# Performance work log

Hardware: AMD Instinct MI355X
Metric: run time of the kernel (lower is better)

The kernel has to match this reference:

```python
import jax, jax.numpy as jnp
import numpy as np

TEMP = 0.07  # module hardcodes self.temp = 0.07 regardless of ctor arg
N, C = 8192, 256


def setup_inputs() -> dict:
    key = jax.random.key(0)
    kq, kk = jax.random.split(key)
    q = jax.random.normal(kq, (N, C), dtype=jnp.float32)
    k = jax.random.normal(kk, (N, C), dtype=jnp.float32)
    return {"q": q, "k": k}


def reference(q, k):
    # Original builds logits = [l_pos, l_neg_row] per sample i where
    # l_pos = q_i . k_i and l_neg_row = q_i . k_j for j != i, then applies
    # CrossEntropyLoss with label 0. That logits row is exactly a permutation
    # of the full similarity row sim[i, :] = q_i @ k.T (diagonal = positive),
    # so CE(logits/T, 0) == logsumexp(sim_i/T) - sim_ii/T. Single fused GEMM
    # + row-wise logsumexp, identical math and gradients.
    sim = jnp.matmul(q, k.T) / TEMP            # [N, N]
    pos = jnp.diagonal(sim)                    # [N]
    lse = jax.nn.logsumexp(sim, axis=1)        # [N]
    return jnp.mean(lse - pos)                 # scalar loss
```

## Files before the change

kernel.cpp:

```cpp
#include <hip/hip_runtime.h>
#include <stdint.h>


#define N_ROWS 8192
#define C_DIM  256
#define BN     32
#define SPLIT  16
#define JCOLS  (N_ROWS / SPLIT)
#define JTILES (JCOLS / BN)
#define BLK_ROWS 128
#define TILE_B  (BN * C_DIM * 2)

typedef __attribute__((ext_vector_type(8)))  _Float16 half8;
typedef __attribute__((ext_vector_type(4)))  _Float16 half4;
typedef __attribute__((ext_vector_type(4)))  float    f32x4;

#if __has_builtin(__builtin_amdgcn_exp2f)
#define EXP2(x) __builtin_amdgcn_exp2f(x)
#else
#define EXP2(x) exp2f(x)
#endif
#if __has_builtin(__builtin_amdgcn_logf)
#define LOG2(x) __builtin_amdgcn_logf(x)
#else
#define LOG2(x) log2f(x)
#endif

__device__ __forceinline__ void gload_lds16(const void* g, void* l) {
  __builtin_amdgcn_global_load_lds(
      (const __attribute__((address_space(1))) unsigned int*)g,
      (__attribute__((address_space(3))) unsigned int*)l, 16, 0, 0);
}

__global__ void cvt_kernel(const float* __restrict__ q, const float* __restrict__ k,
                           _Float16* __restrict__ qh, _Float16* __restrict__ kh,
                           float* __restrict__ pP) {
  const float QS = 20.60992915555663f;
  int i = blockIdx.x * 256 + threadIdx.x;
  float4 qv = ((const float4*)q)[i];
  float4 kv = ((const float4*)k)[i];
  half4 qo, ko;
  qo[0] = (_Float16)(qv.x * QS); qo[1] = (_Float16)(qv.y * QS);
  qo[2] = (_Float16)(qv.z * QS); qo[3] = (_Float16)(qv.w * QS);
  ko[0] = (_Float16)kv.x; ko[1] = (_Float16)kv.y;
  ko[2] = (_Float16)kv.z; ko[3] = (_Float16)kv.w;
  ((half4*)qh)[i] = qo;
  ((half4*)kh)[i] = ko;

  float d = (float)qo[0] * (float)ko[0];
  d = fmaf((float)qo[1], (float)ko[1], d);
  d = fmaf((float)qo[2], (float)ko[2], d);
  d = fmaf((float)qo[3], (float)ko[3], d);
#pragma unroll
  for (int off = 1; off < 64; off <<= 1) d += __shfl_xor(d, off);
  if ((threadIdx.x & 63) == 0) pP[i >> 6] = d;
}

__launch_bounds__(256, 2)
__global__ void sim_lse_kernel(const _Float16* __restrict__ qh,
                               const _Float16* __restrict__ kh,
                               float* __restrict__ pM,
                               float* __restrict__ pS) {
  __shared__ __align__(16) _Float16 kt[2 * BN * C_DIM];
  const int tid  = threadIdx.x;
  const int lane = tid & 63;
  const int wave = tid >> 6;
  const int l15  = lane & 15;
  const int lg   = lane >> 4;

  const int bid  = blockIdx.x;
  const int sp   = bid & (SPLIT - 1);
  const int rb   = bid >> 4;
  const int row0 = rb * BLK_ROWS + wave * 32;

  half8 a[2][8];
#pragma unroll
  for (int rf = 0; rf < 2; ++rf) {
    const _Float16* qr = qh + (size_t)(row0 + rf * 16 + l15) * C_DIM + lg * 8;
#pragma unroll
    for (int ks = 0; ks < 8; ++ks) a[rf][ks] = *(const half8*)(qr + ks * 32);
  }

  float M[8], S[8];
#pragma unroll
  for (int s = 0; s < 8; ++s) { M[s] = -__builtin_inff(); S[s] = 0.f; }

  const int nl0 = l15;
  const int nl1 = 16 + l15;
  const int bb0 = nl0 * 512 + (((nl0 & 31) * 16) ^ (lg * 16));
  const int bb1 = nl1 * 512 + (((nl1 & 31) * 16) ^ (lg * 16));

  const char* ksrc = (const char*)(kh + (size_t)sp * JCOLS * C_DIM);
  char* lds = (char*)kt;

#pragma unroll
  for (int it = 0; it < 4; ++it) {
    int linear = it * 4096 + tid * 16;
    int row = linear >> 9;
    int gc  = ((linear >> 4) & 31) ^ (row & 31);
    gload_lds16(ksrc + row * 512 + gc * 16, lds + linear);
  }

  for (int jt = 0; jt < JTILES; ++jt) {
    __syncthreads();
    const char* cur = lds + (jt & 1) * TILE_B;

    if (jt + 1 < JTILES) {
      const char* src = ksrc + (size_t)(jt + 1) * TILE_B;
      char* nxt = lds + ((jt + 1) & 1) * TILE_B;
#pragma unroll
      for (int it = 0; it < 4; ++it) {
        int linear = it * 4096 + tid * 16;
        int row = linear >> 9;
        int gc  = ((linear >> 4) & 31) ^ (row & 31);
        gload_lds16(src + row * 512 + gc * 16, nxt + linear);
      }
    }

    f32x4 acc00 = {0.f,0.f,0.f,0.f}, acc01 = {0.f,0.f,0.f,0.f};
    f32x4 acc10 = {0.f,0.f,0.f,0.f}, acc11 = {0.f,0.f,0.f,0.f};

#pragma unroll
    for (int ks = 0; ks < 8; ++ks) {
      half8 b0 = *(const half8*)(cur + (bb0 ^ (ks * 64)));
      half8 b1 = *(const half8*)(cur + (bb1 ^ (ks * 64)));
      acc00 = __builtin_amdgcn_mfma_f32_16x16x32_f16(a[0][ks], b0, acc00, 0, 0, 0);
      acc01 = __builtin_amdgcn_mfma_f32_16x16x32_f16(a[0][ks], b1, acc01, 0, 0, 0);
      acc10 = __builtin_amdgcn_mfma_f32_16x16x32_f16(a[1][ks], b0, acc10, 0, 0, 0);
      acc11 = __builtin_amdgcn_mfma_f32_16x16x32_f16(a[1][ks], b1, acc11, 0, 0, 0);
    }

#pragma unroll
    for (int j = 0; j < 4; ++j) {
      {
        float v0 = acc00[j], v1 = acc01[j];
        float newM  = fmaxf(M[j], fmaxf(v0, v1));
        float alpha = EXP2(M[j] - newM);
        float p = EXP2(v0 - newM) + EXP2(v1 - newM);
        S[j] = fmaf(S[j], alpha, p);
        M[j] = newM;
      }
      {
        float v0 = acc10[j], v1 = acc11[j];
        float newM  = fmaxf(M[4 + j], fmaxf(v0, v1));
        float alpha = EXP2(M[4 + j] - newM);
        float p = EXP2(v0 - newM) + EXP2(v1 - newM);
        S[4 + j] = fmaf(S[4 + j], alpha, p);
        M[4 + j] = newM;
      }
    }
  }

#pragma unroll
  for (int s = 0; s < 8; ++s) {
#pragma unroll
    for (int off = 1; off < 16; off <<= 1) {
      float Mo = __shfl_xor(M[s], off);
      float So = __shfl_xor(S[s], off);
      float nm = fmaxf(M[s], Mo);
      S[s] = S[s] * EXP2(M[s] - nm) + So * EXP2(Mo - nm);
      M[s] = nm;
    }
  }

  if (l15 == 0) {
#pragma unroll
    for (int s = 0; s < 8; ++s) {
      int grow = row0 + (s >> 2) * 16 + lg * 4 + (s & 3);
      pM[(size_t)sp * N_ROWS + grow] = M[s];
      pS[(size_t)sp * N_ROWS + grow] = S[s];
    }
  }
}

__global__ void finish1_kernel(const float* __restrict__ pM, const float* __restrict__ pS,
                               const float* __restrict__ pP, float* __restrict__ pPart) {
  const int tid = threadIdx.x;
  const int r = blockIdx.x * 256 + tid;
  float m = -__builtin_inff();
#pragma unroll
  for (int s = 0; s < SPLIT; ++s) m = fmaxf(m, pM[s * N_ROWS + r]);
  float ssum = 0.f;
#pragma unroll
  for (int s = 0; s < SPLIT; ++s)
    ssum = fmaf(pS[s * N_ROWS + r], EXP2(pM[s * N_ROWS + r] - m), ssum);
  float accl = (m + LOG2(ssum)) - pP[r];
#pragma unroll
  for (int off = 1; off < 64; off <<= 1) accl += __shfl_xor(accl, off);
  __shared__ float wsum[4];
  if ((tid & 63) == 0) wsum[tid >> 6] = accl;
  __syncthreads();
  if (tid == 0)
    pPart[blockIdx.x] = wsum[0] + wsum[1] + wsum[2] + wsum[3];
}

__global__ void finish2_kernel(const float* __restrict__ pPart, float* __restrict__ out) {
  const int tid = threadIdx.x;
  float v = (tid < 32) ? pPart[tid] : 0.f;
#pragma unroll
  for (int off = 1; off < 64; off <<= 1) v += __shfl_xor(v, off);
  if (tid == 0)
    out[0] = v * (0.69314718055994531f / (float)N_ROWS);
}

extern "C" void kernel_launch(void* const* d_in, const int* in_sizes, int n_in,
                              void* d_out, int out_size, void* d_ws, size_t ws_size,
                              hipStream_t stream) {
  const float* q = (const float*)d_in[0];
  const float* k = (const float*)d_in[1];
  float* out = (float*)d_out;
  char* ws = (char*)d_ws;

  _Float16* qh = (_Float16*)ws;
  _Float16* kh = (_Float16*)(ws + (size_t)N_ROWS * C_DIM * 2);
  float* pM = (float*)(ws + (size_t)N_ROWS * C_DIM * 4);
  float* pS = pM + SPLIT * N_ROWS;
  float* pP = pS + SPLIT * N_ROWS;
  float* pPart = pP + N_ROWS;

  cvt_kernel<<<dim3(N_ROWS * C_DIM / 4 / 256), dim3(256), 0, stream>>>(q, k, qh, kh, pP);
  sim_lse_kernel<<<dim3((N_ROWS / BLK_ROWS) * SPLIT), dim3(256), 0, stream>>>(qh, kh, pM, pS);
  finish1_kernel<<<dim3(N_ROWS / 256), dim3(256), 0, stream>>>(pM, pS, pP, pPart);
  finish2_kernel<<<dim3(1), dim3(64), 0, stream>>>(pPart, out);
}
```

Measured before the change: 112.6 us.

## Triple-buffer K tiles in LDS with prefetch distance two and partial vmcnt waits

Grows the LDS ring for K tiles from two to three buffers and issues global-to-LDS loads two tiles ahead. Explicit s_waitcnt vmcnt(4) plus a raw s_barrier replace __syncthreads, so each iteration waits only for the oldest tile's loads. The goal is to hide global load latency behind the MFMA and LSE work. LDS use rises from 32KB to 48KB per block, which could cut occupancy below the two blocks per CU the launch bounds request. The hand-written waitcnt is also fragile if the compiler emits other vector memory ops.

```diff
diff --git a/kernel.cpp b/kernel.cpp
--- a/kernel.cpp
+++ b/kernel.cpp
@@ -10,6 +10,7 @@
 #define JTILES (JCOLS / BN)
 #define BLK_ROWS 128
 #define TILE_B  (BN * C_DIM * 2)
+#define NBUF   3
 
 typedef __attribute__((ext_vector_type(8)))  _Float16 half8;
 typedef __attribute__((ext_vector_type(4)))  _Float16 half4;
@@ -61,7 +62,7 @@
                                const _Float16* __restrict__ kh,
                                float* __restrict__ pM,
                                float* __restrict__ pS) {
-  __shared__ __align__(16) _Float16 kt[2 * BN * C_DIM];
+  __shared__ __align__(16) _Float16 kt[NBUF * BN * C_DIM];
   const int tid  = threadIdx.x;
   const int lane = tid & 63;
   const int wave = tid >> 6;
@@ -93,29 +94,38 @@
   const char* ksrc = (const char*)(kh + (size_t)sp * JCOLS * C_DIM);
   char* lds = (char*)kt;
 
-#pragma unroll
-  for (int it = 0; it < 4; ++it) {
-    int linear = it * 4096 + tid * 16;
-    int row = linear >> 9;
-    int gc  = ((linear >> 4) & 31) ^ (row & 31);
-    gload_lds16(ksrc + row * 512 + gc * 16, lds + linear);
-  }
-
+#define STAGE(t, bufidx)                                                     \
+  do {                                                                       \
+    const char* _src = ksrc + (size_t)(t) * TILE_B;                          \
+    char* _dst = lds + (bufidx) * TILE_B;                                    \
+    _Pragma("unroll")                                                        \
+    for (int _it = 0; _it < 4; ++_it) {                                      \
+      int _lin = _it * 4096 + tid * 16;                                      \
+      int _row = _lin >> 9;                                                  \
+      int _gc  = ((_lin >> 4) & 31) ^ (_row & 31);                           \
+      gload_lds16(_src + _row * 512 + _gc * 16, _dst + _lin);                \
+    }                                                                        \
+  } while (0)
+
+  STAGE(0, 0);
+  STAGE(1, 1);
+
+  int cb = 0;
   for (int jt = 0; jt < JTILES; ++jt) {
-    __syncthreads();
-    const char* cur = lds + (jt & 1) * TILE_B;
-
-    if (jt + 1 < JTILES) {
-      const char* src = ksrc + (size_t)(jt + 1) * TILE_B;
-      char* nxt = lds + ((jt + 1) & 1) * TILE_B;
-#pragma unroll
-      for (int it = 0; it < 4; ++it) {
-        int linear = it * 4096 + tid * 16;
-        int row = linear >> 9;
-        int gc  = ((linear >> 4) & 31) ^ (row & 31);
-        gload_lds16(src + row * 512 + gc * 16, nxt + linear);
-      }
-    }
+    if (jt < JTILES - 1) {
+      asm volatile("s_waitcnt vmcnt(4)" ::: "memory");
+    } else {
+      asm volatile("s_waitcnt vmcnt(0)" ::: "memory");
+    }
+    __builtin_amdgcn_sched_barrier(0);
+    __builtin_amdgcn_s_barrier();
+
+    if (jt + 2 < JTILES) {
+      int nb = cb + 2; if (nb >= NBUF) nb -= NBUF;
+      STAGE(jt + 2, nb);
+    }
+
+    const char* cur = lds + cb * TILE_B;
 
     f32x4 acc00 = {0.f,0.f,0.f,0.f}, acc01 = {0.f,0.f,0.f,0.f};
     f32x4 acc10 = {0.f,0.f,0.f,0.f}, acc11 = {0.f,0.f,0.f,0.f};
@@ -149,7 +159,10 @@
         M[4 + j] = newM;
       }
     }
-  }
+
+    ++cb; if (cb >= NBUF) cb -= NBUF;
+  }
+#undef STAGE
 
 #pragma unroll
   for (int s = 0; s < 8; ++s) {
```

Result: no change. 110.9 us (-1.6%).

## Load K tiles directly from global into registers, dropping LDS staging

Applied to the files above, without the earlier changes.

Replaces the double-buffered LDS staging of K tiles (global_load_lds plus __syncthreads) with direct per-wave global half8 loads into registers, each followed by a batch of MFMAs raised in priority with s_setprio. This removes LDS traffic and block-wide barriers. In exchange each of the four waves now fetches the same K data separately from L2/L1 with no prefetch pipelining, so load latency is exposed unless occupancy hides it.

```diff
diff --git a/kernel.cpp b/kernel.cpp
--- a/kernel.cpp
+++ b/kernel.cpp
@@ -25,12 +25,6 @@
 #else
 #define LOG2(x) log2f(x)
 #endif
-
-__device__ __forceinline__ void gload_lds16(const void* g, void* l) {
-  __builtin_amdgcn_global_load_lds(
-      (const __attribute__((address_space(1))) unsigned int*)g,
-      (__attribute__((address_space(3))) unsigned int*)l, 16, 0, 0);
-}
 
 __global__ void cvt_kernel(const float* __restrict__ q, const float* __restrict__ k,
                            _Float16* __restrict__ qh, _Float16* __restrict__ kh,
@@ -61,7 +55,6 @@
                                const _Float16* __restrict__ kh,
                                float* __restrict__ pM,
                                float* __restrict__ pS) {
-  __shared__ __align__(16) _Float16 kt[2 * BN * C_DIM];
   const int tid  = threadIdx.x;
   const int lane = tid & 63;
   const int wave = tid >> 6;
@@ -85,56 +78,45 @@
 #pragma unroll
   for (int s = 0; s < 8; ++s) { M[s] = -__builtin_inff(); S[s] = 0.f; }
 
-  const int nl0 = l15;
-  const int nl1 = 16 + l15;
-  const int bb0 = nl0 * 512 + (((nl0 & 31) * 16) ^ (lg * 16));
-  const int bb1 = nl1 * 512 + (((nl1 & 31) * 16) ^ (lg * 16));
-
-  const char* ksrc = (const char*)(kh + (size_t)sp * JCOLS * C_DIM);
-  char* lds = (char*)kt;
-
-#pragma unroll
-  for (int it = 0; it < 4; ++it) {
-    int linear = it * 4096 + tid * 16;
-    int row = linear >> 9;
-    int gc  = ((linear >> 4) & 31) ^ (row & 31);
-    gload_lds16(ksrc + row * 512 + gc * 16, lds + linear);
-  }
+  const char* kb0 = (const char*)(kh + (size_t)sp * JCOLS * C_DIM)
+                    + l15 * 512 + lg * 16;
+  const char* kb1 = kb0 + 16 * 512;
 
   for (int jt = 0; jt < JTILES; ++jt) {
-    __syncthreads();
-    const char* cur = lds + (jt & 1) * TILE_B;
-
-    if (jt + 1 < JTILES) {
-      const char* src = ksrc + (size_t)(jt + 1) * TILE_B;
-      char* nxt = lds + ((jt + 1) & 1) * TILE_B;
-#pragma unroll
-      for (int it = 0; it < 4; ++it) {
-        int linear = it * 4096 + tid * 16;
-        int row = linear >> 9;
-        int gc  = ((linear >> 4) & 31) ^ (row & 31);
-        gload_lds16(src + row * 512 + gc * 16, nxt + linear);
-      }
-    }
-
     f32x4 acc00 = {0.f,0.f,0.f,0.f}, acc01 = {0.f,0.f,0.f,0.f};
     f32x4 acc10 = {0.f,0.f,0.f,0.f}, acc11 = {0.f,0.f,0.f,0.f};
 
-#pragma unroll
-    for (int ks = 0; ks < 8; ++ks) {
-      half8 b0 = *(const half8*)(cur + (bb0 ^ (ks * 64)));
-      half8 b1 = *(const half8*)(cur + (bb1 ^ (ks * 64)));
-      acc00 = __builtin_amdgcn_mfma_f32_16x16x32_f16(a[0][ks], b0, acc00, 0, 0, 0);
-      acc01 = __builtin_amdgcn_mfma_f32_16x16x32_f16(a[0][ks], b1, acc01, 0, 0, 0);
-      acc10 = __builtin_amdgcn_mfma_f32_16x16x32_f16(a[1][ks], b0, acc10, 0, 0, 0);
-      acc11 = __builtin_amdgcn_mfma_f32_16x16x32_f16(a[1][ks], b1, acc11, 0, 0, 0);
-    }
+    {
+      half8 b[8];
+#pragma unroll
+      for (int ks = 0; ks < 8; ++ks) b[ks] = *(const half8*)(kb0 + ks * 64);
+      __builtin_amdgcn_s_setprio(1);
+#pragma unroll
+      for (int ks = 0; ks < 8; ++ks) {
+        acc00 = __builtin_amdgcn_mfma_f32_16x16x32_f16(a[0][ks], b[ks], acc00, 0, 0, 0);
+        acc10 = __builtin_amdgcn_mfma_f32_16x16x32_f16(a[1][ks], b[ks], acc10, 0, 0, 0);
+      }
+      __builtin_amdgcn_s_setprio(0);
+    }
+    {
+      half8 b[8];
+#pragma unroll
+      for (int ks = 0; ks < 8; ++ks) b[ks] = *(const half8*)(kb1 + ks * 64);
+      __builtin_amdgcn_s_setprio(1);
+#pragma unroll
+      for (int ks = 0; ks < 8; ++ks) {
+        acc01 = __builtin_amdgcn_mfma_f32_16x16x32_f16(a[0][ks], b[ks], acc01, 0, 0, 0);
+        acc11 = __builtin_amdgcn_mfma_f32_16x16x32_f16(a[1][ks], b[ks], acc11, 0, 0, 0);
+      }
+      __builtin_amdgcn_s_setprio(0);
+    }
+    kb0 += TILE_B; kb1 += TILE_B;
 
 #pragma unroll
     for (int j = 0; j < 4; ++j) {
       {
         float v0 = acc00[j], v1 = acc01[j];
-        float newM  = fmaxf(M[j], fmaxf(v0, v1));
+        float newM  = fmaxf(fmaxf(M[j], v0), v1);
         float alpha = EXP2(M[j] - newM);
         float p = EXP2(v0 - newM) + EXP2(v1 - newM);
         S[j] = fmaf(S[j], alpha, p);
@@ -142,7 +124,7 @@
       }
       {
         float v0 = acc10[j], v1 = acc11[j];
-        float newM  = fmaxf(M[4 + j], fmaxf(v0, v1));
+        float newM  = fmaxf(fmaxf(M[4 + j], v0), v1);
         float alpha = EXP2(M[4 + j] - newM);
         float p = EXP2(v0 - newM) + EXP2(v1 - newM);
         S[4 + j] = fmaf(S[4 + j], alpha, p);
```

Measured after the change: 191.6 us. 70.2% more time.
